# Optimization experiments

Hardware: AMD Instinct MI355X
Metric: run time of the kernel (lower is better)

## Reference

```python
import jax, jax.numpy as jnp
import numpy as np

TEMPERATURE = 8.0  # sqrt(head_dim=64)
B, LQ, LK, D = 8, 512, 512, 64


def setup_inputs() -> dict:
    key = jax.random.key(0)
    kq, kk, kv, kb = jax.random.split(key, 4)
    return {
        "q": jax.random.normal(kq, (B, LQ, D), dtype=jnp.float32),
        "k": jax.random.normal(kk, (B, LK, D), dtype=jnp.float32),
        "v": jax.random.normal(kv, (B, LK, D), dtype=jnp.float32),
        "bias": jax.random.normal(kb, (B, LQ, LK, D), dtype=jnp.float32),
    }


def reference(q, k, v, bias):
    # attn1[b,i,j] = q . k ; attn2[b,i,j] = q[b,i] . bias[b,i,j]
    scores = (jnp.einsum('bid,bjd->bij', q, k)
              + jnp.einsum('bid,bijd->bij', q, bias)) / TEMPERATURE
    attn = jax.nn.softmax(scores, axis=2)  # [B, LQ, LK]
    # dropout is identity in eval/deterministic reference
    # emb1 = attn @ v ; emb2[b,i] = sum_j attn[b,i,j] * bias[b,i,j,:]
    output = (jnp.einsum('bij,bjd->bid', attn, v)
              + jnp.einsum('bij,bijd->bid', attn, bias))
    return (output, attn)
```

## Files before the change

### kernel.cpp

```cpp
#include <hip/hip_runtime.h>

#define BB 8
#define LQ 512
#define LK 512
#define DD 64

constexpr float SCALE_LOG2E = 0.125f * 1.44269504088896340736f;

typedef float f32x2 __attribute__((ext_vector_type(2)));
typedef float f32x4 __attribute__((ext_vector_type(4)));

__global__ __launch_bounds__(256) void attn_bias_kernel(
    const float* __restrict__ q,
    const float* __restrict__ k,
    const float* __restrict__ v,
    const float* __restrict__ bias,
    float* __restrict__ out_emb,
    float* __restrict__ out_attn)
{
    const int row  = blockIdx.x;
    const int b    = row >> 9;
    const int tid  = threadIdx.x;
    const int wave = tid >> 6;
    const int lane = tid & 63;
    const int jj   = lane >> 4;
    const int t    = lane & 15;
    const int g    = (wave << 2) | jj;

    __shared__ float s1_lds[LK];
    __shared__ float w_lds[LK];
    __shared__ f32x4 o_lds[16 * 16];
    __shared__ float l_lds[16];

    const f32x4 qf = reinterpret_cast<const f32x4*>(q + row * DD)[t];

    const f32x4* bias_row = reinterpret_cast<const f32x4*>(
        bias + (size_t)row * (LK * DD));
    const f32x4* k_b = reinterpret_cast<const f32x4*>(k + b * (LK * DD));
    const f32x4* v_b = reinterpret_cast<const f32x4*>(v + b * (LK * DD));

    #pragma unroll 4
    for (int it0 = 0; it0 < LK / 16; ++it0) {
        const int it = (it0 + row) & 31;
        const int j  = (it << 4) + g;
        const f32x4 kv = k_b[j * (DD / 4) + t];
        float part = qf.x * kv.x + qf.y * kv.y + qf.z * kv.z + qf.w * kv.w;
        part += __shfl_xor(part, 1);
        part += __shfl_xor(part, 2);
        part += __shfl_xor(part, 4);
        part += __shfl_xor(part, 8);
        if (t == 0) s1_lds[j] = part;
    }
    __syncthreads();

    float l = 0.f;
    f32x4 o = {0.f, 0.f, 0.f, 0.f};

    #pragma unroll 4
    for (int it = 0; it < LK / 16; ++it) {
        const int j = (it << 4) + g;
        const f32x4 bv =
            __builtin_nontemporal_load(&bias_row[j * (DD / 4) + t]);
        float part = qf.x * bv.x + qf.y * bv.y + qf.z * bv.z + qf.w * bv.w;
        part += __shfl_xor(part, 1);
        part += __shfl_xor(part, 2);
        part += __shfl_xor(part, 4);
        part += __shfl_xor(part, 8);
        const float s1j = s1_lds[j];
        const float w = __builtin_amdgcn_exp2f((part + s1j) * SCALE_LOG2E);
        if (t == 0) w_lds[j] = w;
        l += w;
        o.x += w * bv.x;
        o.y += w * bv.y;
        o.z += w * bv.z;
        o.w += w * bv.w;
    }
    __syncthreads();

    #pragma unroll 4
    for (int it0 = 0; it0 < LK / 16; ++it0) {
        const int it = (it0 + row) & 31;
        const int j  = (it << 4) + g;
        const f32x4 vv = v_b[j * (DD / 4) + t];
        const float w  = w_lds[j];
        o.x += w * vv.x;
        o.y += w * vv.y;
        o.z += w * vv.z;
        o.w += w * vv.w;
    }

    o_lds[g * 16 + t] = o;
    if (t == 0) l_lds[g] = l;
    __syncthreads();

    float L = 0.f;
    #pragma unroll
    for (int gg = 0; gg < 16; ++gg) L += l_lds[gg];
    const float invL = 1.0f / L;

    {
        const f32x2* w2 = reinterpret_cast<const f32x2*>(w_lds);
        f32x2* attn_row2 = reinterpret_cast<f32x2*>(
            out_attn + (size_t)row * LK);
        f32x2 val = w2[tid];
        val.x *= invL;
        val.y *= invL;
        __builtin_nontemporal_store(val, &attn_row2[tid]);
    }

    if (tid < DD) {
        const float* o_f = reinterpret_cast<const float*>(o_lds);
        float O = 0.f;
        #pragma unroll
        for (int gg = 0; gg < 16; ++gg)
            O += o_f[gg * DD + tid];
        out_emb[row * DD + tid] = O * invL;
    }
}

extern "C" void kernel_launch(void* const* d_in, const int* in_sizes, int n_in,
                              void* d_out, int out_size, void* d_ws, size_t ws_size,
                              hipStream_t stream) {
    const float* q    = (const float*)d_in[0];
    const float* k    = (const float*)d_in[1];
    const float* v    = (const float*)d_in[2];
    const float* bias = (const float*)d_in[3];
    float* out_emb  = (float*)d_out;
    float* out_attn = (float*)d_out + BB * LQ * DD;

    attn_bias_kernel<<<BB * LQ, 256, 0, stream>>>(q, k, v, bias, out_emb, out_attn);
}
```

Measured before the change: 697.9 us.

## Fuse score, softmax-weight and value passes into one loop with DPP reductions

The three loops over keys (q·k scores, q·bias scores with bias accumulation, then attn·v) are merged into one pass. Each iteration loads bias, k and v together, computes q·(bias+k), and accumulates w·(bias+v). This removes the s1 shared-memory staging and one block barrier. The 16-lane reduction now uses DPP lane permutes in place of xor shuffles, to cut instruction and LDS-path overhead. The cost is more live registers and three concurrent global streams per iteration, which may lower occupancy or change the memory access pattern of the dominant bias stream.

```diff
diff --git a/kernel.cpp b/kernel.cpp
--- a/kernel.cpp
+++ b/kernel.cpp
@@ -9,6 +9,18 @@
 
 typedef float f32x2 __attribute__((ext_vector_type(2)));
 typedef float f32x4 __attribute__((ext_vector_type(4)));
+
+__device__ __forceinline__ float dpp_sum16(float x) {
+    int v = __float_as_int(x);
+    x += __int_as_float(__builtin_amdgcn_update_dpp(0, v, 0xB1, 0xF, 0xF, true));
+    v = __float_as_int(x);
+    x += __int_as_float(__builtin_amdgcn_update_dpp(0, v, 0x4E, 0xF, 0xF, true));
+    v = __float_as_int(x);
+    x += __int_as_float(__builtin_amdgcn_update_dpp(0, v, 0x141, 0xF, 0xF, true));
+    v = __float_as_int(x);
+    x += __int_as_float(__builtin_amdgcn_update_dpp(0, v, 0x140, 0xF, 0xF, true));
+    return x;
+}
 
 __global__ __launch_bounds__(256) void attn_bias_kernel(
     const float* __restrict__ q,
@@ -27,7 +39,6 @@
     const int t    = lane & 15;
     const int g    = (wave << 2) | jj;
 
-    __shared__ float s1_lds[LK];
     __shared__ float w_lds[LK];
     __shared__ f32x4 o_lds[16 * 16];
     __shared__ float l_lds[16];
@@ -39,54 +50,30 @@
     const f32x4* k_b = reinterpret_cast<const f32x4*>(k + b * (LK * DD));
     const f32x4* v_b = reinterpret_cast<const f32x4*>(v + b * (LK * DD));
 
-    #pragma unroll 4
-    for (int it0 = 0; it0 < LK / 16; ++it0) {
-        const int it = (it0 + row) & 31;
-        const int j  = (it << 4) + g;
-        const f32x4 kv = k_b[j * (DD / 4) + t];
-        float part = qf.x * kv.x + qf.y * kv.y + qf.z * kv.z + qf.w * kv.w;
-        part += __shfl_xor(part, 1);
-        part += __shfl_xor(part, 2);
-        part += __shfl_xor(part, 4);
-        part += __shfl_xor(part, 8);
-        if (t == 0) s1_lds[j] = part;
-    }
-    __syncthreads();
-
     float l = 0.f;
     f32x4 o = {0.f, 0.f, 0.f, 0.f};
-
-    #pragma unroll 4
-    for (int it = 0; it < LK / 16; ++it) {
-        const int j = (it << 4) + g;
-        const f32x4 bv =
-            __builtin_nontemporal_load(&bias_row[j * (DD / 4) + t]);
-        float part = qf.x * bv.x + qf.y * bv.y + qf.z * bv.z + qf.w * bv.w;
-        part += __shfl_xor(part, 1);
-        part += __shfl_xor(part, 2);
-        part += __shfl_xor(part, 4);
-        part += __shfl_xor(part, 8);
-        const float s1j = s1_lds[j];
-        const float w = __builtin_amdgcn_exp2f((part + s1j) * SCALE_LOG2E);
-        if (t == 0) w_lds[j] = w;
-        l += w;
-        o.x += w * bv.x;
-        o.y += w * bv.y;
-        o.z += w * bv.z;
-        o.w += w * bv.w;
-    }
-    __syncthreads();
 
     #pragma unroll 4
     for (int it0 = 0; it0 < LK / 16; ++it0) {
         const int it = (it0 + row) & 31;
         const int j  = (it << 4) + g;
+        const f32x4 bv =
+            __builtin_nontemporal_load(&bias_row[j * (DD / 4) + t]);
+        const f32x4 kv = k_b[j * (DD / 4) + t];
         const f32x4 vv = v_b[j * (DD / 4) + t];
-        const float w  = w_lds[j];
-        o.x += w * vv.x;
-        o.y += w * vv.y;
-        o.z += w * vv.z;
-        o.w += w * vv.w;
+
+        float part = qf.x * (bv.x + kv.x) + qf.y * (bv.y + kv.y)
+                   + qf.z * (bv.z + kv.z) + qf.w * (bv.w + kv.w);
+        part = dpp_sum16(part);
+
+        const float w = __builtin_amdgcn_exp2f(part * SCALE_LOG2E);
+        if (t == 0) w_lds[j] = w;
+        l += w;
+
+        o.x += w * (bv.x + vv.x);
+        o.y += w * (bv.y + vv.y);
+        o.z += w * (bv.z + vv.z);
+        o.w += w * (bv.w + vv.w);
     }
 
     o_lds[g * 16 + t] = o;
```

New measurement: 702.9 us. About the same (+0.7%).
